# Optimization experiments

Measured on AMD Instinct MI355X. Metric: run time of the kernel, lower is better.

The kernel has to match this reference:

```python
import jax, jax.numpy as jnp
import numpy as np

D = 768; H = 12; HEAD = 6; SD = 64; S1 = SD * (HEAD - 1); S2 = SD * HEAD
HID = 3072; B = 8; N = 1024
SCALE = (D // H) ** -0.5
EPS = 1e-5


def _ln(x, g, b):
    m = jnp.mean(x, axis=-1, keepdims=True)
    v = jnp.var(x, axis=-1, keepdims=True)
    return (x - m) * jax.lax.rsqrt(v + EPS) * g + b


def setup_inputs() -> dict:
    key = jax.random.key(0)
    ks = jax.random.split(key, 20)
    p = lambda k, shape, s=0.02: (jax.random.normal(k, shape, dtype=jnp.float32) * s)
    return {
        "x": jax.random.normal(ks[0], (B, N, D), dtype=jnp.float32),
        # norm1 / norm12 / norm13 (pre-attention split LayerNorms)
        "ln1a_g": jnp.ones((S1,), jnp.float32), "ln1a_b": jnp.zeros((S1,), jnp.float32),
        "ln1b_g": jnp.ones((SD,), jnp.float32), "ln1b_b": jnp.zeros((SD,), jnp.float32),
        "ln1c_g": jnp.ones((D - S2,), jnp.float32), "ln1c_b": jnp.zeros((D - S2,), jnp.float32),
        # norm2 / norm22 / norm23 (pre-MLP split LayerNorms)
        "ln2a_g": jnp.ones((S1,), jnp.float32), "ln2a_b": jnp.zeros((S1,), jnp.float32),
        "ln2b_g": jnp.ones((SD,), jnp.float32), "ln2b_b": jnp.zeros((SD,), jnp.float32),
        "ln2c_g": jnp.ones((D - S2,), jnp.float32), "ln2c_b": jnp.zeros((D - S2,), jnp.float32),
        # attention (qkv has no bias since qkv_bias=False)
        "qkv_w": p(ks[1], (3 * D, D)),
        "proj_w": p(ks[2], (D, D)), "proj_b": jnp.zeros((D,), jnp.float32),
        # mlp
        "fc1_w": p(ks[3], (HID, D)), "fc1_b": jnp.zeros((HID,), jnp.float32),
        "fc2_w": p(ks[4], (D, HID)), "fc2_b": jnp.zeros((D,), jnp.float32),
    }


def _split_norm(x, ga, ba, gb, bb, gc, bc):
    return jnp.concatenate([
        _ln(x[:, :, :S1], ga, ba),
        _ln(x[:, :, S1:S2], gb, bb),
        _ln(x[:, :, S2:], gc, bc),
    ], axis=2)


def _attention(x, qkv_w, proj_w, proj_b):
    Bq, Nq, C = x.shape
    hd = C // H
    qkv = jnp.einsum('bnc,dc->bnd', x, qkv_w)  # [B,N,3C]
    qkv = qkv.reshape(Bq, Nq, 3, H, hd).transpose(2, 0, 3, 1, 4)
    q, k, v = qkv[0], qkv[1], qkv[2]  # [B,H,N,hd]
    attn = jax.nn.softmax(jnp.einsum('bhqd,bhkd->bhqk', q, k) * SCALE, axis=-1)
    y = jnp.einsum('bhqk,bhkd->bhqd', attn, v)  # [B,H,N,hd]
    y = y.transpose(0, 2, 1, 3).reshape(Bq, Nq, C)
    return jnp.einsum('bnc,dc->bnd', y, proj_w) + proj_b


def reference(x, ln1a_g, ln1a_b, ln1b_g, ln1b_b, ln1c_g, ln1c_b,
              ln2a_g, ln2a_b, ln2b_g, ln2b_b, ln2c_g, ln2c_b,
              qkv_w, proj_w, proj_b, fc1_w, fc1_b, fc2_w, fc2_b):
    norm_x = _split_norm(x, ln1a_g, ln1a_b, ln1b_g, ln1b_b, ln1c_g, ln1c_b)
    x = x + _attention(norm_x, qkv_w, proj_w, proj_b)
    norm2_x = _split_norm(x, ln2a_g, ln2a_b, ln2b_g, ln2b_b, ln2c_g, ln2c_b)
    h = jax.nn.gelu(jnp.einsum('bnc,hc->bnh', norm2_x, fc1_w) + fc1_b, approximate=False)
    x = x + (jnp.einsum('bnh,ch->bnc', h, fc2_w) + fc2_b)
    return x
```

## Files before the change

### kernel.cpp

```cpp
#include <hip/hip_runtime.h>
#include <math.h>

#define NTOK 8192
#define DIM 768
#define SEQ 1024
#define NH 12
#define HD 64
#define HID 3072
#define S1V 320
#define S2V 384

typedef unsigned short bfu;
typedef __attribute__((ext_vector_type(8))) short short8;
typedef __attribute__((ext_vector_type(4))) float f32x4;

__device__ __forceinline__ bfu f2bf(float f){
  unsigned int u = __float_as_uint(f);
  u += 0x7FFFu + ((u >> 16) & 1u);
  return (bfu)(u >> 16);
}
__device__ __forceinline__ f32x4 mfma16(short8 a, short8 b, f32x4 c){
  return __builtin_amdgcn_mfma_f32_16x16x32_bf16(a, b, c, 0, 0, 0);
}
__device__ __forceinline__ void gll16(const void* g, void* l){
  __builtin_amdgcn_global_load_lds(
      (const __attribute__((address_space(1))) unsigned int*)g,
      (__attribute__((address_space(3))) unsigned int*)l, 16, 0, 0);
}
__device__ __forceinline__ int swz(int a){ return a ^ (((a >> 7) & 7) << 4); }
__device__ __forceinline__ int swz2(int a){ return a ^ (((a >> 7) & 7) << 4); }

__global__ __launch_bounds__(256) void cvt_kernel(const float4* __restrict__ src,
                                                  ushort4* __restrict__ dst, int n4){
  for (int i = blockIdx.x * 256 + threadIdx.x; i < n4; i += gridDim.x * 256){
    float4 f = src[i];
    ushort4 o;
    o.x = f2bf(f.x); o.y = f2bf(f.y); o.z = f2bf(f.z); o.w = f2bf(f.w);
    dst[i] = o;
  }
}

__global__ __launch_bounds__(256) void ln_split(
    const float* __restrict__ x,
    const float* __restrict__ ga, const float* __restrict__ ba,
    const float* __restrict__ gb, const float* __restrict__ bb2,
    const float* __restrict__ gc, const float* __restrict__ bc,
    bfu* __restrict__ out)
{
  const int row = blockIdx.x, t = threadIdx.x;
  const float* xr = x + (size_t)row * DIM;
  const float e0 = xr[t], e1 = xr[t + 256], e2 = xr[t + 512];
  float s0 = e0, q0 = e0 * e0, s1 = 0.f, q1 = 0.f, s2 = e2, q2 = e2 * e2;
  const int i1 = t + 256;
  if (i1 < S1V)      { s0 += e1; q0 += e1 * e1; }
  else if (i1 < S2V) { s1 += e1; q1 += e1 * e1; }
  else               { s2 += e1; q2 += e1 * e1; }
  float v[6] = {s0, q0, s1, q1, s2, q2};
  #pragma unroll
  for (int k = 0; k < 6; ++k)
    #pragma unroll
    for (int off = 32; off; off >>= 1)
      v[k] += __shfl_xor(v[k], off);
  __shared__ float red[6][4];
  const int lane = t & 63, wave = t >> 6;
  if (lane == 0){
    #pragma unroll
    for (int k = 0; k < 6; ++k) red[k][wave] = v[k];
  }
  __syncthreads();
  float tt[6];
  #pragma unroll
  for (int k = 0; k < 6; ++k) tt[k] = red[k][0] + red[k][1] + red[k][2] + red[k][3];
  const float m0 = tt[0] * (1.f/320.f);
  const float r0 = rsqrtf(tt[1] * (1.f/320.f) - m0*m0 + 1e-5f);
  const float m1 = tt[2] * (1.f/64.f);
  const float r1 = rsqrtf(tt[3] * (1.f/64.f) - m1*m1 + 1e-5f);
  const float m2 = tt[4] * (1.f/384.f);
  const float r2 = rsqrtf(tt[5] * (1.f/384.f) - m2*m2 + 1e-5f);
  bfu* orow = out + (size_t)row * DIM;
  orow[t] = f2bf((e0 - m0) * r0 * ga[t] + ba[t]);
  {
    float ov;
    if (i1 < S1V)      ov = (e1 - m0) * r0 * ga[i1] + ba[i1];
    else if (i1 < S2V) ov = (e1 - m1) * r1 * gb[i1 - S1V] + bb2[i1 - S1V];
    else               ov = (e1 - m2) * r2 * gc[i1 - S2V] + bc[i1 - S2V];
    orow[i1] = f2bf(ov);
  }
  const int i2 = t + 512;
  orow[i2] = f2bf((e2 - m2) * r2 * gc[i2 - S2V] + bc[i2 - S2V]);
}

template<int BIAS, int GELU_, int RESID, int OUTF32, int QSC, int SPLITK>
__global__ __launch_bounds__(512, 2) void gemm256(
    const bfu* __restrict__ A, const bfu* __restrict__ Bw,
    int N, int ldK, int ntn,
    const float* __restrict__ bias, const float* __restrict__ resid,
    float* __restrict__ outf, bfu* __restrict__ outb)
{
  __shared__ __align__(16) char lds[2][2][32768];
  const int tid = threadIdx.x;
  const int lane = tid & 63;
  const int wave = tid >> 6;
  const int wm = wave >> 2, wn = wave & 3;
  const int r = lane & 15, g = lane >> 4;
  const int sx = (r & 7) << 4;

  const int nwg = gridDim.x, cpx = nwg >> 3;
  const int sb = (blockIdx.x & 7) * cpx + (blockIdx.x >> 3);
  const int per = 32 * ntn;
  const int kg  = SPLITK ? (sb / per) : 0;
  const int rem = SPLITK ? (sb % per) : sb;
  const int tm = rem / ntn, tn = rem % ntn;

  const int Kloc = SPLITK ? (ldK >> 1) : ldK;
  const size_t ld2 = (size_t)ldK * 2;
  const size_t koff2 = (size_t)kg * Kloc * 2;

  f32x4 acc[8][4];
  #pragma unroll
  for (int i = 0; i < 8; ++i)
    #pragma unroll
    for (int j = 0; j < 4; ++j) acc[i][j] = (f32x4){0.f, 0.f, 0.f, 0.f};

  const int Ls = swz2(tid * 16);
  const int r0 = Ls >> 7;
  const int c0 = Ls & 127;
  const char* Abase = (const char*)A + (size_t)tm * 256 * ld2 + koff2 + c0;
  const char* Bbase = (const char*)Bw + (size_t)tn * 256 * ld2 + koff2 + c0;
  const int tid16 = tid * 16;

  const int nt = Kloc >> 6;

  #define STAGE(b, t) do { \
    const char* Ao = Abase + (size_t)(t) * 128; \
    const char* Bo = Bbase + (size_t)(t) * 128; \
    _Pragma("unroll") \
    for (int is = 0; is < 4; ++is) \
      gll16(Ao + (size_t)(is * 64 + r0) * ld2, &lds[b][0][is * 8192 + tid16]); \
    _Pragma("unroll") \
    for (int is = 0; is < 4; ++is) \
      gll16(Bo + (size_t)(is * 64 + r0) * ld2, &lds[b][1][is * 8192 + tid16]); \
  } while (0)

  STAGE(0, 0);
  STAGE(1, 1);
  asm volatile("s_waitcnt vmcnt(8)" ::: "memory");
  __builtin_amdgcn_s_barrier();

  for (int t = 0; t < nt; ++t){
    const int cur = t & 1;
    const char* lA = lds[cur][0];
    const char* lB = lds[cur][1];
    short8 bfr[4][2];
    #pragma unroll
    for (int n = 0; n < 4; ++n)
      #pragma unroll
      for (int h = 0; h < 2; ++h)
        bfr[n][h] = *(const short8*)(lB + ((((wn * 64 + n * 16 + r) * 128) + h * 64 + g * 16) ^ sx));
    #pragma unroll
    for (int mp = 0; mp < 4; ++mp){
      short8 afr[2][2];
      #pragma unroll
      for (int mm = 0; mm < 2; ++mm)
        #pragma unroll
        for (int h = 0; h < 2; ++h)
          afr[mm][h] = *(const short8*)(lA + ((((wm * 128 + (mp * 2 + mm) * 16 + r) * 128) + h * 64 + g * 16) ^ sx));
      __builtin_amdgcn_s_setprio(1);
      #pragma unroll
      for (int mm = 0; mm < 2; ++mm)
        #pragma unroll
        for (int n = 0; n < 4; ++n){
          acc[mp * 2 + mm][n] = mfma16(afr[mm][0], bfr[n][0], acc[mp * 2 + mm][n]);
          acc[mp * 2 + mm][n] = mfma16(afr[mm][1], bfr[n][1], acc[mp * 2 + mm][n]);
        }
      __builtin_amdgcn_s_setprio(0);
    }
    asm volatile("s_waitcnt vmcnt(0)" ::: "memory");
    __builtin_amdgcn_s_barrier();
    if (t + 2 < nt) STAGE(cur, t + 2);
  }
  #undef STAGE

  const int row0 = tm * 256 + wm * 128;
  const int col0 = tn * 256 + wn * 64;
  #pragma unroll
  for (int n = 0; n < 4; ++n){
    const int colb = col0 + n * 16 + r;
    const float bi = (BIAS && (!SPLITK || kg == 0)) ? bias[colb] : 0.f;
    #pragma unroll
    for (int m = 0; m < 8; ++m){
      #pragma unroll
      for (int q = 0; q < 4; ++q){
        const int rowg = row0 + m * 16 + g * 4 + q;
        float v = acc[m][n][q] + bi;
        if (GELU_) v = 0.5f * v * (1.f + erff(v * 0.70710678118654752440f));
        if (QSC && colb < 768) v *= 0.125f;
        const size_t idx = (size_t)rowg * N + colb;
        if (SPLITK){
          atomicAdd(&outf[idx], v);
        } else {
          if (RESID) v += resid[idx];
          if (OUTF32) outf[idx] = v;
          else        outb[idx] = f2bf(v);
        }
      }
    }
  }
}

__global__ __launch_bounds__(256) void vtrans(const bfu* __restrict__ qkv, bfu* __restrict__ vt){
  __shared__ bfu tile[64][66];
  const int bh = blockIdx.x, kt = blockIdx.y;
  const int b = bh / NH, h = bh - b * NH;
  const int tid = threadIdx.x;
  const int tr = tid >> 5;
  const int tc = (tid & 31) * 2;
  #pragma unroll
  for (int pass = 0; pass < 8; ++pass){
    const int k = pass * 8 + tr;
    const bfu* src = qkv + (size_t)(b * SEQ + kt * 64 + k) * 2304 + 1536 + h * 64 + tc;
    tile[k][tc] = src[0]; tile[k][tc + 1] = src[1];
  }
  __syncthreads();
  #pragma unroll
  for (int pass = 0; pass < 8; ++pass){
    const int d = pass * 8 + tr;
    bfu* dst = vt + ((size_t)bh * 64 + d) * SEQ + kt * 64 + tc;
    dst[0] = tile[tc][d]; dst[1] = tile[tc + 1][d];
  }
}

__global__ __launch_bounds__(512) void attn2(
    const bfu* __restrict__ qkv, const bfu* __restrict__ vt, bfu* __restrict__ y)
{
  __shared__ __align__(16) char kbuf[2][8192];
  __shared__ __align__(16) char vbuf[2][8192];
  __shared__ __align__(16) char plds_all[8][2048];
  const int tid = threadIdx.x, lane = tid & 63, wave = tid >> 6;
  char* plds = plds_all[wave];
  const int blk = blockIdx.x;
  const int bh = blk >> 3, q128 = blk & 7;
  const int b = bh / NH, h = bh - b * NH;
  const int r = lane & 15, g = lane >> 4;

  const bfu* qbase = qkv + (size_t)(b * SEQ + q128 * 128 + wave * 16 + r) * 2304 + h * 64;
  const short8 qf0 = *(const short8*)(qbase + g * 8);
  const short8 qf1 = *(const short8*)(qbase + 32 + g * 8);

  const int P = tid * 16;
  const int Ls = swz(P);
  const int srow = Ls >> 7, scol = Ls & 127;
  const char* kg = (const char*)(qkv + (size_t)(b * SEQ) * 2304 + 768 + h * 64)
                   + (size_t)srow * 4608 + scol;
  const char* vg = (const char*)(vt + (size_t)bh * 64 * SEQ)
                   + (size_t)srow * 2048 + scol;

  int off[4][2];
  #pragma unroll
  for (int f = 0; f < 4; ++f){
    off[f][0] = swz((f * 16 + r) * 128 + g * 16);
    off[f][1] = swz((f * 16 + r) * 128 + 64 + g * 16);
  }

  float m_[4], l_[4];
  f32x4 yacc[4];
  #pragma unroll
  for (int i = 0; i < 4; ++i){ m_[i] = -1e30f; l_[i] = 0.f; yacc[i] = (f32x4){0.f,0.f,0.f,0.f}; }

  gll16(kg, &kbuf[0][P]);
  gll16(vg, &vbuf[0][P]);
  __syncthreads();

  for (int kt = 0; kt < 16; ++kt){
    const int cur = kt & 1;
    if (kt + 1 < 16){
      gll16(kg + (size_t)(kt + 1) * 294912, &kbuf[cur ^ 1][P]);
      gll16(vg + (kt + 1) * 128, &vbuf[cur ^ 1][P]);
    }
    const char* lK = kbuf[cur];
    const char* lV = vbuf[cur];

    f32x4 s[4];
    #pragma unroll
    for (int c = 0; c < 4; ++c){
      const short8 kf0 = *(const short8*)(lK + off[c][0]);
      const short8 kf1 = *(const short8*)(lK + off[c][1]);
      s[c] = (f32x4){0.f, 0.f, 0.f, 0.f};
      s[c] = mfma16(qf0, kf0, s[c]);
      s[c] = mfma16(qf1, kf1, s[c]);
    }
    float pm[4];
    #pragma unroll
    for (int q = 0; q < 4; ++q)
      pm[q] = fmaxf(fmaxf(s[0][q], s[1][q]), fmaxf(s[2][q], s[3][q]));
    #pragma unroll
    for (int q = 0; q < 4; ++q)
      #pragma unroll
      for (int o = 1; o < 16; o <<= 1)
        pm[q] = fmaxf(pm[q], __shfl_xor(pm[q], o));
    float rs[4];
    #pragma unroll
    for (int q = 0; q < 4; ++q){
      const float mn = fmaxf(m_[q], pm[q]);
      const float al = __expf(m_[q] - mn);
      m_[q] = mn;
      l_[q] *= al;
      #pragma unroll
      for (int f = 0; f < 4; ++f) yacc[f][q] *= al;
      float acc = 0.f;
      #pragma unroll
      for (int c = 0; c < 4; ++c){
        const float p = __expf(s[c][q] - mn);
        s[c][q] = p;
        acc += p;
      }
      rs[q] = acc;
    }
    #pragma unroll
    for (int q = 0; q < 4; ++q){
      #pragma unroll
      for (int o = 1; o < 16; o <<= 1)
        rs[q] += __shfl_xor(rs[q], o);
      l_[q] += rs[q];
    }
    #pragma unroll
    for (int c = 0; c < 4; ++c)
      #pragma unroll
      for (int q = 0; q < 4; ++q){
        const int a = swz((g * 4 + q) * 128 + (c * 16 + r) * 2);
        *(bfu*)&plds[a] = f2bf(s[c][q]);
      }
    short8 pa[2];
    #pragma unroll
    for (int ks = 0; ks < 2; ++ks)
      pa[ks] = *(const short8*)&plds[swz(r * 128 + ks * 64 + g * 16)];
    #pragma unroll
    for (int f = 0; f < 4; ++f){
      const short8 vf0 = *(const short8*)(lV + off[f][0]);
      const short8 vf1 = *(const short8*)(lV + off[f][1]);
      yacc[f] = mfma16(pa[0], vf0, yacc[f]);
      yacc[f] = mfma16(pa[1], vf1, yacc[f]);
    }
    __syncthreads();
  }

  bfu* yb = y + (size_t)(b * SEQ + q128 * 128 + wave * 16) * DIM + h * 64;
  #pragma unroll
  for (int f = 0; f < 4; ++f)
    #pragma unroll
    for (int q = 0; q < 4; ++q)
      yb[(size_t)(g * 4 + q) * DIM + f * 16 + r] = f2bf(yacc[f][q] / l_[q]);
}

extern "C" void kernel_launch(void* const* d_in, const int* in_sizes, int n_in,
                              void* d_out, int out_size, void* d_ws, size_t ws_size,
                              hipStream_t stream) {
  const float* x      = (const float*)d_in[0];
  const float* ln1ag  = (const float*)d_in[1];
  const float* ln1ab  = (const float*)d_in[2];
  const float* ln1bg  = (const float*)d_in[3];
  const float* ln1bb  = (const float*)d_in[4];
  const float* ln1cg  = (const float*)d_in[5];
  const float* ln1cb  = (const float*)d_in[6];
  const float* ln2ag  = (const float*)d_in[7];
  const float* ln2ab  = (const float*)d_in[8];
  const float* ln2bg  = (const float*)d_in[9];
  const float* ln2bb  = (const float*)d_in[10];
  const float* ln2cg  = (const float*)d_in[11];
  const float* ln2cb  = (const float*)d_in[12];
  const float* qkv_w  = (const float*)d_in[13];
  const float* proj_w = (const float*)d_in[14];
  const float* proj_b = (const float*)d_in[15];
  const float* fc1_w  = (const float*)d_in[16];
  const float* fc1_b  = (const float*)d_in[17];
  const float* fc2_w  = (const float*)d_in[18];
  const float* fc2_b  = (const float*)d_in[19];
  float* outp = (float*)d_out;

  char* ws = (char*)d_ws;
  bfu* wqkv   = (bfu*)(ws + 0);
  bfu* wproj  = (bfu*)(ws + 3538944);
  bfu* wfc1   = (bfu*)(ws + 4718592);
  bfu* wfc2   = (bfu*)(ws + 9437184);
  bfu* lnbuf  = (bfu*)(ws + 14155776);
  bfu* ybuf   = (bfu*)(ws + 26738688);
  bfu* qkvbuf = (bfu*)(ws + 39321600);
  bfu* vtbuf  = (bfu*)(ws + 77070336);
  bfu* hbuf   = qkvbuf;

  cvt_kernel<<<512, 256, 0, stream>>>((const float4*)qkv_w,  (ushort4*)wqkv, 2304*768/4);
  cvt_kernel<<<256, 256, 0, stream>>>((const float4*)proj_w, (ushort4*)wproj, 768*768/4);
  cvt_kernel<<<512, 256, 0, stream>>>((const float4*)fc1_w,  (ushort4*)wfc1, 3072*768/4);
  cvt_kernel<<<512, 256, 0, stream>>>((const float4*)fc2_w,  (ushort4*)wfc2, 768*3072/4);

  ln_split<<<NTOK, 256, 0, stream>>>(x, ln1ag, ln1ab, ln1bg, ln1bb, ln1cg, ln1cb, lnbuf);
  gemm256<0,0,0,0,1,0><<<288, 512, 0, stream>>>(lnbuf, wqkv, 2304, 768, 9,
                                                nullptr, nullptr, nullptr, qkvbuf);
  vtrans<<<dim3(96,16), 256, 0, stream>>>(qkvbuf, vtbuf);
  attn2<<<768, 512, 0, stream>>>(qkvbuf, vtbuf, ybuf);
  gemm256<1,0,1,1,0,0><<<96, 512, 0, stream>>>(ybuf, wproj, 768, 768, 3,
                                               proj_b, x, outp, nullptr);
  ln_split<<<NTOK, 256, 0, stream>>>(outp, ln2ag, ln2ab, ln2bg, ln2bb, ln2cg, ln2cb, lnbuf);
  gemm256<1,1,0,0,0,0><<<384, 512, 0, stream>>>(lnbuf, wfc1, 3072, 768, 12,
                                                fc1_b, nullptr, nullptr, hbuf);
  gemm256<1,0,0,0,0,1><<<192, 512, 0, stream>>>(hbuf, wfc2, 768, 3072, 3,
                                                fc2_b, nullptr, outp, nullptr);
}
```

Measured before the change: 503.3 us.

## Interleave GEMM global loads with MFMA phases and drop split-K for fc2

The GEMM main loop is split into four compute phases, and each half-tile global-to-LDS load is issued between them instead of staging whole tiles after the compute. Partial vmcnt waits and extra barriers let loads overlap MFMA work. The split-K atomic path for fc2 is removed; fc2 now runs 96 blocks with full K=3072 and adds the residual in place from outp. Dropping split-K removes the atomics but halves the block count for fc2 on a large GPU, and the added barriers cost some synchronisation.

After: 520.5 us. 3.4% more time.

```diff
diff --git a/kernel.cpp b/kernel.cpp
--- a/kernel.cpp
+++ b/kernel.cpp
@@ -90,10 +90,10 @@
   orow[i2] = f2bf((e2 - m2) * r2 * gc[i2 - S2V] + bc[i2 - S2V]);
 }
 
-template<int BIAS, int GELU_, int RESID, int OUTF32, int QSC, int SPLITK>
-__global__ __launch_bounds__(512, 2) void gemm256(
+template<int BIAS, int GELU_, int RESID, int OUTF32, int QSC>
+__global__ __launch_bounds__(512, 2) void gemm8p(
     const bfu* __restrict__ A, const bfu* __restrict__ Bw,
-    int N, int ldK, int ntn,
+    int N, int K, int ntn,
     const float* __restrict__ bias, const float* __restrict__ resid,
     float* __restrict__ outf, bfu* __restrict__ outb)
 {
@@ -107,14 +107,9 @@
 
   const int nwg = gridDim.x, cpx = nwg >> 3;
   const int sb = (blockIdx.x & 7) * cpx + (blockIdx.x >> 3);
-  const int per = 32 * ntn;
-  const int kg  = SPLITK ? (sb / per) : 0;
-  const int rem = SPLITK ? (sb % per) : sb;
-  const int tm = rem / ntn, tn = rem % ntn;
-
-  const int Kloc = SPLITK ? (ldK >> 1) : ldK;
-  const size_t ld2 = (size_t)ldK * 2;
-  const size_t koff2 = (size_t)kg * Kloc * 2;
+  const int tm = sb / ntn, tn = sb % ntn;
+
+  const size_t ld2 = (size_t)K * 2;
 
   f32x4 acc[8][4];
   #pragma unroll
@@ -125,68 +120,90 @@
   const int Ls = swz2(tid * 16);
   const int r0 = Ls >> 7;
   const int c0 = Ls & 127;
-  const char* Abase = (const char*)A + (size_t)tm * 256 * ld2 + koff2 + c0;
-  const char* Bbase = (const char*)Bw + (size_t)tn * 256 * ld2 + koff2 + c0;
+  const char* Abase = (const char*)A + (size_t)tm * 256 * ld2 + c0;
+  const char* Bbase = (const char*)Bw + (size_t)tn * 256 * ld2 + c0;
   const int tid16 = tid * 16;
-
-  const int nt = Kloc >> 6;
-
-  #define STAGE(b, t) do { \
-    const char* Ao = Abase + (size_t)(t) * 128; \
-    const char* Bo = Bbase + (size_t)(t) * 128; \
+  const int nt = K >> 6;
+
+  #define SHALF(mx, slt, h, t) do { \
+    const char* gb = ((mx) ? Bbase : Abase) + (size_t)(t) * 128; \
     _Pragma("unroll") \
-    for (int is = 0; is < 4; ++is) \
-      gll16(Ao + (size_t)(is * 64 + r0) * ld2, &lds[b][0][is * 8192 + tid16]); \
+    for (int j = 0; j < 2; ++j) \
+      gll16(gb + (size_t)(((h) * 2 + j) * 64 + r0) * ld2, \
+            &lds[slt][mx][((h) * 2 + j) * 8192 + tid16]); \
+  } while (0)
+
+  #define LDA(lA, p) do { \
     _Pragma("unroll") \
-    for (int is = 0; is < 4; ++is) \
-      gll16(Bo + (size_t)(is * 64 + r0) * ld2, &lds[b][1][is * 8192 + tid16]); \
+    for (int mm = 0; mm < 2; ++mm) \
+      _Pragma("unroll") \
+      for (int h2 = 0; h2 < 2; ++h2) \
+        afr[mm][h2] = *(const short8*)((lA) + ((((wm * 128 + ((p) * 2 + mm) * 16 + r) * 128) + h2 * 64 + g * 16) ^ sx)); \
   } while (0)
 
-  STAGE(0, 0);
-  STAGE(1, 1);
-  asm volatile("s_waitcnt vmcnt(8)" ::: "memory");
-  __builtin_amdgcn_s_barrier();
+  #define MM(p) do { \
+    __builtin_amdgcn_s_setprio(1); \
+    _Pragma("unroll") \
+    for (int mm = 0; mm < 2; ++mm) \
+      _Pragma("unroll") \
+      for (int n = 0; n < 4; ++n){ \
+        acc[(p) * 2 + mm][n] = mfma16(afr[mm][0], bfr[n][0], acc[(p) * 2 + mm][n]); \
+        acc[(p) * 2 + mm][n] = mfma16(afr[mm][1], bfr[n][1], acc[(p) * 2 + mm][n]); \
+      } \
+    __builtin_amdgcn_s_setprio(0); \
+  } while (0)
+
+  SHALF(0, 0, 0, 0); SHALF(0, 0, 1, 0); SHALF(1, 0, 0, 0); SHALF(1, 0, 1, 0);
+  SHALF(0, 1, 0, 1); SHALF(0, 1, 1, 1); SHALF(1, 1, 0, 1); SHALF(1, 1, 1, 1);
 
   for (int t = 0; t < nt; ++t){
-    const int cur = t & 1;
-    const char* lA = lds[cur][0];
-    const char* lB = lds[cur][1];
+    const int s = t & 1;
+    if (t == 0)            asm volatile("s_waitcnt vmcnt(8)" ::: "memory");
+    else if (t + 1 < nt)   asm volatile("s_waitcnt vmcnt(4)" ::: "memory");
+    else                   asm volatile("s_waitcnt vmcnt(0)" ::: "memory");
+    __builtin_amdgcn_sched_barrier(0);
+    __builtin_amdgcn_s_barrier();
+
+    const char* lA = lds[s][0];
+    const char* lB = lds[s][1];
     short8 bfr[4][2];
+    short8 afr[2][2];
+
     #pragma unroll
     for (int n = 0; n < 4; ++n)
       #pragma unroll
-      for (int h = 0; h < 2; ++h)
-        bfr[n][h] = *(const short8*)(lB + ((((wn * 64 + n * 16 + r) * 128) + h * 64 + g * 16) ^ sx));
-    #pragma unroll
-    for (int mp = 0; mp < 4; ++mp){
-      short8 afr[2][2];
-      #pragma unroll
-      for (int mm = 0; mm < 2; ++mm)
-        #pragma unroll
-        for (int h = 0; h < 2; ++h)
-          afr[mm][h] = *(const short8*)(lA + ((((wm * 128 + (mp * 2 + mm) * 16 + r) * 128) + h * 64 + g * 16) ^ sx));
-      __builtin_amdgcn_s_setprio(1);
-      #pragma unroll
-      for (int mm = 0; mm < 2; ++mm)
-        #pragma unroll
-        for (int n = 0; n < 4; ++n){
-          acc[mp * 2 + mm][n] = mfma16(afr[mm][0], bfr[n][0], acc[mp * 2 + mm][n]);
-          acc[mp * 2 + mm][n] = mfma16(afr[mm][1], bfr[n][1], acc[mp * 2 + mm][n]);
-        }
-      __builtin_amdgcn_s_setprio(0);
-    }
-    asm volatile("s_waitcnt vmcnt(0)" ::: "memory");
-    __builtin_amdgcn_s_barrier();
-    if (t + 2 < nt) STAGE(cur, t + 2);
-  }
-  #undef STAGE
+      for (int h2 = 0; h2 < 2; ++h2)
+        bfr[n][h2] = *(const short8*)(lB + ((((wn * 64 + n * 16 + r) * 128) + h2 * 64 + g * 16) ^ sx));
+    LDA(lA, 0);
+    if (t >= 1 && t + 1 < nt) SHALF(0, s ^ 1, 0, t + 1);
+    __builtin_amdgcn_s_barrier();
+    MM(0);
+    __builtin_amdgcn_s_barrier();
+    LDA(lA, 1);
+    if (t >= 1 && t + 1 < nt) SHALF(0, s ^ 1, 1, t + 1);
+    __builtin_amdgcn_s_barrier();
+    MM(1);
+    __builtin_amdgcn_s_barrier();
+    LDA(lA, 2);
+    if (t + 2 < nt) SHALF(1, s, 0, t + 2);
+    __builtin_amdgcn_s_barrier();
+    MM(2);
+    __builtin_amdgcn_s_barrier();
+    LDA(lA, 3);
+    if (t + 2 < nt) SHALF(1, s, 1, t + 2);
+    __builtin_amdgcn_s_barrier();
+    MM(3);
+  }
+  #undef SHALF
+  #undef LDA
+  #undef MM
 
   const int row0 = tm * 256 + wm * 128;
   const int col0 = tn * 256 + wn * 64;
   #pragma unroll
   for (int n = 0; n < 4; ++n){
     const int colb = col0 + n * 16 + r;
-    const float bi = (BIAS && (!SPLITK || kg == 0)) ? bias[colb] : 0.f;
+    const float bi = BIAS ? bias[colb] : 0.f;
     #pragma unroll
     for (int m = 0; m < 8; ++m){
       #pragma unroll
@@ -196,13 +213,10 @@
         if (GELU_) v = 0.5f * v * (1.f + erff(v * 0.70710678118654752440f));
         if (QSC && colb < 768) v *= 0.125f;
         const size_t idx = (size_t)rowg * N + colb;
-        if (SPLITK){
-          atomicAdd(&outf[idx], v);
-        } else {
-          if (RESID) v += resid[idx];
-          if (OUTF32) outf[idx] = v;
-          else        outb[idx] = f2bf(v);
-        }
+        float vv = v;
+        if (RESID) vv += resid[idx];
+        if (OUTF32) outf[idx] = vv;
+        else        outb[idx] = f2bf(vv);
       }
     }
   }
@@ -394,15 +408,15 @@
   cvt_kernel<<<512, 256, 0, stream>>>((const float4*)fc2_w,  (ushort4*)wfc2, 768*3072/4);
 
   ln_split<<<NTOK, 256, 0, stream>>>(x, ln1ag, ln1ab, ln1bg, ln1bb, ln1cg, ln1cb, lnbuf);
-  gemm256<0,0,0,0,1,0><<<288, 512, 0, stream>>>(lnbuf, wqkv, 2304, 768, 9,
-                                                nullptr, nullptr, nullptr, qkvbuf);
+  gemm8p<0,0,0,0,1><<<288, 512, 0, stream>>>(lnbuf, wqkv, 2304, 768, 9,
+                                             nullptr, nullptr, nullptr, qkvbuf);
   vtrans<<<dim3(96,16), 256, 0, stream>>>(qkvbuf, vtbuf);
   attn2<<<768, 512, 0, stream>>>(qkvbuf, vtbuf, ybuf);
-  gemm256<1,0,1,1,0,0><<<96, 512, 0, stream>>>(ybuf, wproj, 768, 768, 3,
-                                               proj_b, x, outp, nullptr);
+  gemm8p<1,0,1,1,0><<<96, 512, 0, stream>>>(ybuf, wproj, 768, 768, 3,
+                                            proj_b, x, outp, nullptr);
   ln_split<<<NTOK, 256, 0, stream>>>(outp, ln2ag, ln2ab, ln2bg, ln2bb, ln2cg, ln2cb, lnbuf);
-  gemm256<1,1,0,0,0,0><<<384, 512, 0, stream>>>(lnbuf, wfc1, 3072, 768, 12,
-                                                fc1_b, nullptr, nullptr, hbuf);
-  gemm256<1,0,0,0,0,1><<<192, 512, 0, stream>>>(hbuf, wfc2, 768, 3072, 3,
-                                                fc2_b, nullptr, outp, nullptr);
-}
+  gemm8p<1,1,0,0,0><<<384, 512, 0, stream>>>(lnbuf, wfc1, 3072, 768, 12,
+                                             fc1_b, nullptr, nullptr, hbuf);
+  gemm8p<1,0,1,1,0><<<96, 512, 0, stream>>>(hbuf, wfc2, 768, 3072, 3,
+                                            fc2_b, outp, outp, nullptr);
+}
```
